# Kernel optimization log

Hardware: AMD Instinct MI355X
Metric: run time of the kernel (lower is better)

## Reference

```python
import jax, jax.numpy as jnp
import numpy as np

NEG_SLOPE = 0.2

def gat_conv(x, src, dst, W, a_src, a_dst, b, num_nodes, concat):
    # PyG GATConv (add_self_loops already applied to src/dst).
    H, C = a_src.shape
    h = (x @ W).reshape(-1, H, C)                      # [N,H,C]
    s = jnp.einsum('nhc,hc->nh', h, a_src)             # per-node src score
    d = jnp.einsum('nhc,hc->nh', h, a_dst)             # per-node dst score
    e = jax.nn.leaky_relu(s[src] + d[dst], NEG_SLOPE)  # [E,H]
    emax = jax.lax.stop_gradient(
        jax.ops.segment_max(e, dst, num_segments=num_nodes))  # [N,H]
    ex = jnp.exp(e - emax[dst])
    denom = jax.ops.segment_sum(ex, dst, num_segments=num_nodes)
    alpha = ex / denom[dst]                            # segment softmax over in-edges
    msg = h[src] * alpha[:, :, None]                   # [E,H,C]
    out = jax.ops.segment_sum(msg, dst, num_segments=num_nodes)
    out = out.reshape(num_nodes, H * C) if concat else out.mean(axis=1)
    return out + b

def setup_inputs() -> dict:
    key = jax.random.key(0)
    ks = jax.random.split(key, 20)
    N, E, F = 50000, 400000, 256
    x = jax.random.normal(ks[0], (N, F), dtype=jnp.float32)
    edge_index = jax.random.randint(ks[1], (2, E), 0, N, dtype=jnp.int64)
    def p(k, shape):
        return (jax.random.normal(k, shape, dtype=jnp.float32) * 0.1)
    inp = {'x': x, 'edge_index': edge_index}
    # conv1: 256 -> 8x32 ; conv2: 256 -> 4x32 ; conv3: 128 -> 2x32 ; conv4: 64 -> 1x32
    dims = [(256, 8, 32), (256, 4, 32), (128, 2, 32), (64, 1, 32)]
    ki = 2
    for i, (fin, H, C) in enumerate(dims, start=1):
        inp[f'W{i}'] = p(ks[ki], (fin, H * C)); ki += 1
        inp[f'a_src{i}'] = p(ks[ki], (H, C)); ki += 1
        inp[f'a_dst{i}'] = p(ks[ki], (H, C)); ki += 1
        bdim = H * C if i < 4 else C
        inp[f'b{i}'] = jnp.zeros((bdim,), dtype=jnp.float32)
    return inp

def reference(x, edge_index, W1, a_src1, a_dst1, b1, W2, a_src2, a_dst2, b2,
              W3, a_src3, a_dst3, b3, W4, a_src4, a_dst4, b4):
    N = x.shape[0]
    loops = jnp.arange(N, dtype=edge_index.dtype)
    src = jnp.concatenate([edge_index[0], loops])
    dst = jnp.concatenate([edge_index[1], loops])
    h = jax.nn.elu(gat_conv(x, src, dst, W1, a_src1, a_dst1, b1, N, True))
    h = jax.nn.elu(gat_conv(h, src, dst, W2, a_src2, a_dst2, b2, N, True))
    h = gat_conv(h, src, dst, W3, a_src3, a_dst3, b3, N, True)
    h = jax.nn.elu(h)
    h = gat_conv(h, src, dst, W4, a_src4, a_dst4, b4, N, False)
    return jax.nn.log_softmax(h, axis=1)
```

## Files before the change

### kernel.cpp

```cpp
#include <hip/hip_runtime.h>
#include <hip/hip_bf16.h>

#define LRELU_SLOPE 0.2f
#define WTOT 108544

typedef __attribute__((ext_vector_type(8))) short short8;
typedef __attribute__((ext_vector_type(4))) float f32x4;

__device__ __forceinline__ unsigned short bf16r(float f) {
    unsigned int u = __builtin_bit_cast(unsigned int, f);
    u += 0x7fffu + ((u >> 16) & 1u);
    return (unsigned short)(u >> 16);
}
__device__ __forceinline__ float bf2f(unsigned short u) {
    return __builtin_bit_cast(float, (unsigned int)u << 16);
}

#define GLD16(g, l)                                                            \
    __builtin_amdgcn_global_load_lds(                                          \
        (const __attribute__((address_space(1))) void*)(g),                    \
        (__attribute__((address_space(3))) void*)(l), 16, 0, 0)

#define QB(v, k) __builtin_amdgcn_ds_swizzle((v), 0x8000 | ((k) * 0x55))


__global__ void k_pre(const float* __restrict__ x, unsigned short* __restrict__ Xb,
                      const float* __restrict__ Wa, const float* __restrict__ Wb,
                      const float* __restrict__ Wc, const float* __restrict__ Wd,
                      unsigned short* __restrict__ Ta, unsigned short* __restrict__ Tb,
                      unsigned short* __restrict__ Tc, unsigned short* __restrict__ Td,
                      const int* __restrict__ ei, int* __restrict__ cnt,
                      int* __restrict__ slot, int XC, int E) {
    int gid = blockIdx.x * blockDim.x + threadIdx.x;
    if (gid < XC) {
        const float4* xp = (const float4*)x + (long)gid * 2;
        float4 a = xp[0], b = xp[1];
        short8 pk;
        pk[0] = (short)bf16r(a.x); pk[1] = (short)bf16r(a.y);
        pk[2] = (short)bf16r(a.z); pk[3] = (short)bf16r(a.w);
        pk[4] = (short)bf16r(b.x); pk[5] = (short)bf16r(b.y);
        pk[6] = (short)bf16r(b.z); pk[7] = (short)bf16r(b.w);
        *(short8*)(Xb + (long)gid * 8) = pk;
        return;
    }
    int id = gid - XC;
    if (id < WTOT) {
        const float* W; unsigned short* T; int K, Nc;
        if (id < 65536)       { W = Wa; T = Ta; K = 256; Nc = 256; }
        else if (id < 98304)  { id -= 65536;  W = Wb; T = Tb; K = 256; Nc = 128; }
        else if (id < 106496) { id -= 98304;  W = Wc; T = Tc; K = 128; Nc = 64; }
        else                  { id -= 106496; W = Wd; T = Td; K = 64;  Nc = 32; }
        int n = id / K, k = id % K;
        T[id] = bf16r(W[(long)k * Nc + n]);
        return;
    }
    int e = id - WTOT;
    if (e >= E) return;
    int dst = ei[E + e];
    slot[e] = atomicAdd(&cnt[dst], 1);
}


__global__ void k_scan_blk(const int* __restrict__ cnt, int* __restrict__ offsR,
                           int* __restrict__ bsum, int* __restrict__ bpre,
                           int* __restrict__ done, int N, int NB) {
    __shared__ int temp[1024];
    __shared__ int last_s;
    int t = threadIdx.x;
    int gi = blockIdx.x * 1024 + t;
    int v = (gi < N) ? cnt[gi] + 1 : 0;
    temp[t] = v;
    __syncthreads();
    for (int o = 1; o < 1024; o <<= 1) {
        int x = (t >= o) ? temp[t - o] : 0;
        __syncthreads();
        temp[t] += x;
        __syncthreads();
    }
    if (gi < N) offsR[gi] = temp[t] - v;
    if (t == 1023) bsum[blockIdx.x] = temp[1023];
    if (t == 0) {
        __threadfence();
        last_s = (atomicAdd(done, 1) == NB - 1) ? 1 : 0;
    }
    __syncthreads();
    if (last_s) {
        __threadfence();
        int v2 = (t < NB) ? bsum[t] : 0;
        temp[t] = v2;
        __syncthreads();
        for (int o = 1; o < 1024; o <<= 1) {
            int x = (t >= o) ? temp[t - o] : 0;
            __syncthreads();
            temp[t] += x;
            __syncthreads();
        }
        if (t < NB) bpre[t] = temp[t] - v2;
        if (t == NB - 1) bpre[NB] = temp[t];
    }
}


__global__ __launch_bounds__(256) void k_mg0fin(
        const int* __restrict__ ei, const int* __restrict__ offsR,
        const int* __restrict__ bpre, const int* __restrict__ slot,
        int* __restrict__ offs, int* __restrict__ adj, int NB, int E,
        const unsigned short* __restrict__ Ab, const unsigned short* __restrict__ WT,
        unsigned short* __restrict__ Cb,
        const float* __restrict__ a_src, const float* __restrict__ a_dst,
        float* __restrict__ sbuf, float* __restrict__ dbuf,
        int M, int RB) {
    constexpr int KT = 256, BN = 64, GX = 4, KH = 128, NR = 2;
    constexpr int KITER = KH / 32;
    constexpr int NBF = BN / 16;
    constexpr int CPR = BN / 32;
    constexpr int SP  = BN + 8;
    constexpr int ASH = 64 * KH;
    constexpr int CHR = KH / 8;
    constexpr int SHC = 4;
    constexpr int AIT = CHR / 4;
    constexpr int BIT = BN * CHR / 256;
    __shared__ __align__(16) unsigned short LB[16384];

    {
        int gtid = blockIdx.x * 256 + threadIdx.x;
        int GT = gridDim.x * 256;
        int N = M;
        int NA = (N + 256) & ~255;
        for (int gi = gtid; gi < NA + E; gi += GT) {
            if (gi < NA) {
                if (gi < N) {
                    int v = offsR[gi] + bpre[gi >> 10];
                    offs[gi] = v;
                    adj[v] = gi;
                } else if (gi == N) {
                    offs[N] = bpre[NB];
                }
            } else {
                int e = gi - NA;
                int dst = ei[E + e];
                adj[offsR[dst] + bpre[dst >> 10] + 1 + slot[e]] = ei[e];
            }
        }
    }

    int id = blockIdx.x;
    int xcd = id & 7;
    int q  = id >> 3;
    int ct = q % GX;
    int rb = (q / GX) * 8 + xcd;
    if (rb >= RB) return;
    int bm = rb * 64, bn = ct * BN;

    int t = threadIdx.x;
    int wv = t >> 6, l = t & 63;
    int row_in = l & 15, quad = l >> 4;
    char* LBb = (char*)LB;
    const char* Agb = (const char*)Ab;
    const char* WTb = (const char*)WT;

    f32x4 acc[NBF];
#pragma unroll
    for (int j = 0; j < NBF; ++j) acc[j] = (f32x4){0.f, 0.f, 0.f, 0.f};

    int arow = wv * 16 + row_in;

#pragma unroll
    for (int r = 0; r < NR; ++r) {
        if (r > 0) __syncthreads();
#pragma unroll
        for (int i = 0; i < AIT; ++i) {
            int c = i * 256 + t;
            int row = c >> SHC;
            int ci  = c & (CHR - 1);
            int cis = ci ^ (row & 7);
            int grow = bm + row; if (grow >= M) grow = M - 1;
            long gb = (long)grow * (KT * 2) + r * (KH * 2) + cis * 16;
            GLD16(Agb + gb, LBb + (i * 256 + wv * 64) * 16);
        }
#pragma unroll
        for (int i = 0; i < BIT; ++i) {
            int c = i * 256 + t;
            int col = c >> SHC;
            int ci  = c & (CHR - 1);
            int cis = ci ^ (col & 7);
            long gb = (long)(bn + col) * (KT * 2) + r * (KH * 2) + cis * 16;
            GLD16(WTb + gb, LBb + ASH * 2 + (i * 256 + wv * 64) * 16);
        }
        asm volatile("s_waitcnt vmcnt(0)" ::: "memory");
        __syncthreads();

#pragma unroll
        for (int ki = 0; ki < KITER; ++ki) {
            int aoff = (arow * (KH * 2) + ki * 64 + quad * 16) ^ ((arow & 7) << 4);
            short8 av = *(const short8*)(LBb + aoff);
#pragma unroll
            for (int f = 0; f < NBF; ++f) {
                int bcol = f * 16 + row_in;
                int boff = ASH * 2 + ((bcol * (KH * 2) + ki * 64 + quad * 16) ^ ((bcol & 7) << 4));
                short8 bv = *(const short8*)(LBb + boff);
                acc[f] = __builtin_amdgcn_mfma_f32_16x16x32_bf16(av, bv, acc[f], 0, 0, 0);
            }
        }
    }
    __syncthreads();

#pragma unroll
    for (int r = 0; r < 4; ++r)
#pragma unroll
        for (int f = 0; f < NBF; ++f)
            LB[(wv * 16 + quad * 4 + r) * SP + f * 16 + row_in] = bf16r(acc[f][r]);
    __syncthreads();

    int rr = t / CPR, cc = t % CPR;
    if (rr < 64) {
        int grow = bm + rr;
        int colb = bn + cc * 32;
        if (grow < M) {
            const unsigned short* ep = &LB[rr * SP + cc * 32];
            short8 v0 = *(const short8*)(ep);
            short8 v1 = *(const short8*)(ep + 8);
            short8 v2 = *(const short8*)(ep + 16);
            short8 v3 = *(const short8*)(ep + 24);
            unsigned short* cp = &Cb[(long)grow * 256 + colb];
            *(short8*)(cp)      = v0;
            *(short8*)(cp + 8)  = v1;
            *(short8*)(cp + 16) = v2;
            *(short8*)(cp + 24) = v3;
            int hd = colb >> 5;
            const float* ap = a_src + hd * 32;
            const float* dp = a_dst + hd * 32;
            float ss = 0.f, dd = 0.f;
#pragma unroll
            for (int u = 0; u < 8; ++u) {
                float va = bf2f((unsigned short)v0[u]); ss += va * ap[u];      dd += va * dp[u];
                float vb = bf2f((unsigned short)v1[u]); ss += vb * ap[8 + u];  dd += vb * dp[8 + u];
                float vc = bf2f((unsigned short)v2[u]); ss += vc * ap[16 + u]; dd += vc * dp[16 + u];
                float vd = bf2f((unsigned short)v3[u]); ss += vd * ap[24 + u]; dd += vd * dp[24 + u];
            }
            sbuf[(long)grow * 8 + hd] = ss;
            dbuf[(long)grow * 8 + hd] = dd;
        }
    }
}


template<int HIN, int NC, int KH>
__global__ __launch_bounds__(256, 4) void k_agmg(
        const unsigned short* __restrict__ h,
        const float* __restrict__ s, const float* __restrict__ dsc,
        const int* __restrict__ offs, const int* __restrict__ adj,
        const float* __restrict__ bias,
        const unsigned short* __restrict__ WT,
        unsigned short* __restrict__ Cb,
        const float* __restrict__ a_src, const float* __restrict__ a_dst,
        float* __restrict__ sb2, float* __restrict__ db2,
        int N, int RB) {
    constexpr int KT   = HIN * 32;
    constexpr int NR   = KT / KH;
    constexpr int KITER = KH / 32;
    constexpr int NBF  = NC / 16;
    constexpr int CPR  = NC / 32;
    constexpr int SP   = NC + 8;
    constexpr int ASH2 = 64 * KT * 2;
    constexpr int CHR  = KH / 8;
    constexpr int BIT  = NC * CHR / 256;
    constexpr int HOUT = NC / 32;
    constexpr int TOT1 = ASH2 + NC * KH * 2;
    constexpr int TOT2 = 64 * SP * 2;
    __shared__ __align__(16) unsigned short LB[(TOT1 > TOT2 ? TOT1 : TOT2) / 2];

    int rb = blockIdx.x;
    if (rb >= RB) return;
    int bm = rb * 64;
    int t = threadIdx.x;
    char* LBb = (char*)LB;

    constexpr int UNITS = 64 * HIN * 4;
    for (int u = t; u < UNITS; u += 256) {
        int c8 = u & 3;
        int hh = (u >> 2) % HIN;
        int nl = u / (4 * HIN);
        int n0 = bm + nl;
        int nn = n0 < N ? n0 : N - 1;
        int beg = offs[nn], end = offs[nn + 1];
        float dn = dsc[nn * HIN + hh];
        int coff = hh * 32 + c8 * 8;
        const unsigned short* hb = h + coff;

        float denom = 0.f;
        float acc[8];
#pragma unroll
        for (int z = 0; z < 8; ++z) acc[z] = 0.f;

        for (int j = beg; j < end; j += 8) {
            int my0 = j + c8;
            int my1 = my0 + 4;
            int i0 = my0 < end ? my0 : end - 1;
            int i1 = my1 < end ? my1 : end - 1;
            int p  = adj[i0];
            int qn = adj[i1];
            int a0 = QB(p, 0),  a1 = QB(p, 1),  a2 = QB(p, 2),  a3 = QB(p, 3);
            int b0 = QB(qn, 0), b1 = QB(qn, 1), b2 = QB(qn, 2), b3 = QB(qn, 3);
            short8 h0 = *(const short8*)(hb + (size_t)a0 * KT);
            short8 h1 = *(const short8*)(hb + (size_t)a1 * KT);
            short8 h2 = *(const short8*)(hb + (size_t)a2 * KT);
            short8 h3 = *(const short8*)(hb + (size_t)a3 * KT);
            short8 h4 = *(const short8*)(hb + (size_t)b0 * KT);
            short8 h5 = *(const short8*)(hb + (size_t)b1 * KT);
            short8 h6 = *(const short8*)(hb + (size_t)b2 * KT);
            short8 h7 = *(const short8*)(hb + (size_t)b3 * KT);
            float e0 = s[p * HIN + hh] + dn;
            float e1 = s[qn * HIN + hh] + dn;
            e0 = e0 > 0.f ? e0 : LRELU_SLOPE * e0;
            e1 = e1 > 0.f ? e1 : LRELU_SLOPE * e1;
            float wA = __expf(fminf(e0, 80.f));
            float wB = __expf(fminf(e1, 80.f));
            if (my0 >= end) wA = 0.f;
            if (my1 >= end) wB = 0.f;
            int wiA = __builtin_bit_cast(int, wA);
            int wiB = __builtin_bit_cast(int, wB);
            float w0 = __builtin_bit_cast(float, QB(wiA, 0));
            float w1 = __builtin_bit_cast(float, QB(wiA, 1));
            float w2 = __builtin_bit_cast(float, QB(wiA, 2));
            float w3 = __builtin_bit_cast(float, QB(wiA, 3));
            float w4 = __builtin_bit_cast(float, QB(wiB, 0));
            float w5 = __builtin_bit_cast(float, QB(wiB, 1));
            float w6 = __builtin_bit_cast(float, QB(wiB, 2));
            float w7 = __builtin_bit_cast(float, QB(wiB, 3));
            denom += ((w0 + w1) + (w2 + w3)) + ((w4 + w5) + (w6 + w7));
#pragma unroll
            for (int z = 0; z < 8; ++z) {
                float aa = w0 * bf2f((unsigned short)h0[z]) + w1 * bf2f((unsigned short)h1[z]);
                float ab = w2 * bf2f((unsigned short)h2[z]) + w3 * bf2f((unsigned short)h3[z]);
                float ac = w4 * bf2f((unsigned short)h4[z]) + w5 * bf2f((unsigned short)h5[z]);
                float ad = w6 * bf2f((unsigned short)h6[z]) + w7 * bf2f((unsigned short)h7[z]);
                acc[z] += (aa + ab) + (ac + ad);
            }
        }

        float inv = 1.0f / denom;
        short8 pk;
#pragma unroll
        for (int z = 0; z < 8; ++z) {
            float o = acc[z] * inv + bias[coff + z];
            float v = o > 0.f ? o : (__expf(o) - 1.f);
            pk[z] = (short)bf16r(v);
        }
        int lbyte = (nl * (KT * 2) + coff * 2) ^ ((nl & 7) << 4);
        *(short8*)(LBb + lbyte) = pk;
    }
    __syncthreads();

    int wv = t >> 6, l = t & 63;
    int row_in = l & 15, quad = l >> 4;
    int arow = wv * 16 + row_in;
    const char* WTb = (const char*)WT;

    f32x4 gac[NBF];
#pragma unroll
    for (int j = 0; j < NBF; ++j) gac[j] = (f32x4){0.f, 0.f, 0.f, 0.f};

#pragma unroll
    for (int r = 0; r < NR; ++r) {
        if (r > 0) __syncthreads();
#pragma unroll
        for (int i = 0; i < BIT; ++i) {
            int c = i * 256 + t;
            int col = c / CHR;
            int ci  = c % CHR;
            int cis = ci ^ (col & 7);
            long gb = (long)col * (KT * 2) + r * (KH * 2) + cis * 16;
            GLD16(WTb + gb, LBb + ASH2 + (i * 256 + wv * 64) * 16);
        }
        asm volatile("s_waitcnt vmcnt(0)" ::: "memory");
        __syncthreads();

#pragma unroll
        for (int ki = 0; ki < KITER; ++ki) {
            int aoff = (arow * (KT * 2) + r * (KH * 2) + ki * 64 + quad * 16) ^ ((arow & 7) << 4);
            short8 av = *(const short8*)(LBb + aoff);
#pragma unroll
            for (int f = 0; f < NBF; ++f) {
                int bcol = f * 16 + row_in;
                int boff = ASH2 + ((bcol * (KH * 2) + ki * 64 + quad * 16) ^ ((bcol & 7) << 4));
                short8 bv = *(const short8*)(LBb + boff);
                gac[f] = __builtin_amdgcn_mfma_f32_16x16x32_bf16(av, bv, gac[f], 0, 0, 0);
            }
        }
    }
    __syncthreads();

#pragma unroll
    for (int r4 = 0; r4 < 4; ++r4)
#pragma unroll
        for (int f = 0; f < NBF; ++f)
            LB[(wv * 16 + quad * 4 + r4) * SP + f * 16 + row_in] = bf16r(gac[f][r4]);
    __syncthreads();

    int rr = t / CPR, cc = t % CPR;
    if (rr < 64) {
        int grow = bm + rr;
        int colb = cc * 32;
        if (grow < N) {
            const unsigned short* ep = &LB[rr * SP + colb];
            short8 v0 = *(const short8*)(ep);
            short8 v1 = *(const short8*)(ep + 8);
            short8 v2 = *(const short8*)(ep + 16);
            short8 v3 = *(const short8*)(ep + 24);
            unsigned short* cp = &Cb[(long)grow * NC + colb];
            *(short8*)(cp)      = v0;
            *(short8*)(cp + 8)  = v1;
            *(short8*)(cp + 16) = v2;
            *(short8*)(cp + 24) = v3;
            int hd = colb >> 5;
            const float* ap = a_src + hd * 32;
            const float* dp = a_dst + hd * 32;
            float ss = 0.f, dd = 0.f;
#pragma unroll
            for (int u = 0; u < 8; ++u) {
                float va = bf2f((unsigned short)v0[u]); ss += va * ap[u];      dd += va * dp[u];
                float vb = bf2f((unsigned short)v1[u]); ss += vb * ap[8 + u];  dd += vb * dp[8 + u];
                float vc = bf2f((unsigned short)v2[u]); ss += vc * ap[16 + u]; dd += vc * dp[16 + u];
                float vd = bf2f((unsigned short)v3[u]); ss += vd * ap[24 + u]; dd += vd * dp[24 + u];
            }
            sb2[(long)grow * HOUT + hd] = ss;
            db2[(long)grow * HOUT + hd] = dd;
        }
    }
}


__global__ void k_aggf_fin(const unsigned short* __restrict__ h, const float* __restrict__ s,
                           const float* __restrict__ dsc, const int* __restrict__ offs,
                           const int* __restrict__ adj, const float* __restrict__ bias,
                           float* __restrict__ out32, int N) {
    const int H = 1, C8 = 4, HC = 32;
    long tid = (long)blockIdx.x * blockDim.x + threadIdx.x;
    if (tid >= (long)N * C8) return;
    int c8 = (int)(tid % C8);
    int n  = (int)(tid / C8);
    int beg = offs[n], end = offs[n + 1];
    float dn = dsc[n * H];
    int coff = c8 * 8;
    const unsigned short* hb = h + coff;

    float denom = 0.f;
    float acc[8];
#pragma unroll
    for (int u = 0; u < 8; ++u) acc[u] = 0.f;

    for (int j = beg; j < end; j += 4) {
        int my = j + c8;
        int idx = my < end ? my : end - 1;
        int sn = adj[idx];
        float e = s[sn * H] + dn;
        e = e > 0.f ? e : LRELU_SLOPE * e;
        float w = __expf(fminf(e, 80.f));
        if (my >= end) w = 0.f;
        int wi = __builtin_bit_cast(int, w);
        int sn0 = QB(sn, 0);
        int sn1 = QB(sn, 1);
        int sn2 = QB(sn, 2);
        int sn3 = QB(sn, 3);
        float w0 = __builtin_bit_cast(float, QB(wi, 0));
        float w1 = __builtin_bit_cast(float, QB(wi, 1));
        float w2 = __builtin_bit_cast(float, QB(wi, 2));
        float w3 = __builtin_bit_cast(float, QB(wi, 3));
        short8 h0 = *(const short8*)(hb + (size_t)sn0 * HC);
        short8 h1 = *(const short8*)(hb + (size_t)sn1 * HC);
        short8 h2 = *(const short8*)(hb + (size_t)sn2 * HC);
        short8 h3 = *(const short8*)(hb + (size_t)sn3 * HC);
        denom += (w0 + w1) + (w2 + w3);
#pragma unroll
        for (int u = 0; u < 8; ++u) {
            float a01 = w0 * bf2f((unsigned short)h0[u]) + w1 * bf2f((unsigned short)h1[u]);
            float a23 = w2 * bf2f((unsigned short)h2[u]) + w3 * bf2f((unsigned short)h3[u]);
            acc[u] += a01 + a23;
        }
    }

    float inv = 1.0f / denom;
    float o[8];
#pragma unroll
    for (int u = 0; u < 8; ++u) o[u] = acc[u] * inv + bias[coff + u];

    float m = o[0];
#pragma unroll
    for (int u = 1; u < 8; ++u) m = fmaxf(m, o[u]);
    m = fmaxf(m, __shfl_xor(m, 1));
    m = fmaxf(m, __shfl_xor(m, 2));
    float ssum = 0.f;
#pragma unroll
    for (int u = 0; u < 8; ++u) ssum += __expf(o[u] - m);
    ssum += __shfl_xor(ssum, 1);
    ssum += __shfl_xor(ssum, 2);
    float lse = m + __logf(ssum);
    float4 lo = {o[0] - lse, o[1] - lse, o[2] - lse, o[3] - lse};
    float4 hi = {o[4] - lse, o[5] - lse, o[6] - lse, o[7] - lse};
    *(float4*)(out32 + tid * 8)     = lo;
    *(float4*)(out32 + tid * 8 + 4) = hi;
}


static inline size_t align_up(size_t x) { return (x + 255) & ~(size_t)255; }

extern "C" void kernel_launch(void* const* d_in, const int* in_sizes, int n_in,
                              void* d_out, int out_size, void* d_ws, size_t ws_size,
                              hipStream_t stream) {
    const float* x   = (const float*)d_in[0];
    const int*   ei  = (const int*)d_in[1];

    const int N = in_sizes[0] / 256;
    const int E = in_sizes[1] / 2;
    const int ET = E + N;
    const int NB = (N + 1023) / 1024;
    const int XC = N * 32;

    size_t off = 0;
    char* ws = (char*)d_ws;
    auto take = [&](size_t bytes) { char* p = ws + off; off += align_up(bytes); return p; };
    int*   cntd  = (int*)take((size_t)(N + 1) * 4);
    int*   offs  = (int*)take((size_t)(N + 1) * 4);
    int*   offsR = (int*)take((size_t)(N + 1) * 4);
    int*   slot  = (int*)take((size_t)E * 4);
    int*   adj   = (int*)take((size_t)ET * 4);
    int*   bsum  = (int*)take((size_t)(NB + 1) * 4);
    int*   bpre  = (int*)take((size_t)(NB + 1) * 4);
    float* s0    = (float*)take((size_t)N * 8 * 4);
    float* d0    = (float*)take((size_t)N * 8 * 4);
    float* s1    = (float*)take((size_t)N * 4 * 4);
    float* d1    = (float*)take((size_t)N * 4 * 4);
    unsigned short* Xb = (unsigned short*)take((size_t)N * 256 * 2);
    unsigned short* Y0 = (unsigned short*)take((size_t)N * 256 * 2);
    unsigned short* Y1 = (unsigned short*)take((size_t)N * 128 * 2);
    unsigned short* WT0 = (unsigned short*)take((size_t)256 * 256 * 2);
    unsigned short* WT1 = (unsigned short*)take((size_t)256 * 128 * 2);
    unsigned short* WT2 = (unsigned short*)take((size_t)128 * 64 * 2);
    unsigned short* WT3 = (unsigned short*)take((size_t)64 * 32 * 2);
    (void)ws_size;

    int* cnt  = cntd;
    int* done = cntd + N;

    const float* as_[4] = {(const float*)d_in[3], (const float*)d_in[7],
                           (const float*)d_in[11], (const float*)d_in[15]};
    const float* ad_[4] = {(const float*)d_in[4], (const float*)d_in[8],
                           (const float*)d_in[12], (const float*)d_in[16]};
    const float* b_[4]  = {(const float*)d_in[5], (const float*)d_in[9],
                           (const float*)d_in[13], (const float*)d_in[17]};

    const int RB  = (N + 63) / 64;
    const int RBp = ((RB + 7) / 8) * 8;

    hipMemsetAsync(cntd, 0, (size_t)(N + 1) * 4, stream);
    {
        long tot = (long)XC + WTOT + E;
        k_pre<<<(int)((tot + 255) / 256), 256, 0, stream>>>(
            x, Xb,
            (const float*)d_in[2], (const float*)d_in[6], (const float*)d_in[10],
            (const float*)d_in[14], WT0, WT1, WT2, WT3, ei, cnt, slot, XC, E);
    }
    k_scan_blk<<<NB, 1024, 0, stream>>>(cnt, offsR, bsum, bpre, done, N, NB);
    k_mg0fin<<<4 * RBp, 256, 0, stream>>>(
        ei, offsR, bpre, slot, offs, adj, NB, E,
        Xb, WT0, Y0, as_[0], ad_[0], s0, d0, N, RB);
    k_agmg<8, 128, 64><<<RB, 256, 0, stream>>>(
        Y0, s0, d0, offs, adj, b_[0], WT1, Y1, as_[1], ad_[1], s1, d1, N, RB);
    k_agmg<4, 64, 128><<<RB, 256, 0, stream>>>(
        Y1, s1, d1, offs, adj, b_[1], WT2, Y0, as_[2], ad_[2], s0, d0, N, RB);
    k_agmg<2, 32, 64><<<RB, 256, 0, stream>>>(
        Y0, s0, d0, offs, adj, b_[2], WT3, Y1, as_[3], ad_[3], s1, d1, N, RB);
    k_aggf_fin<<<(int)(((long)N * 4 + 255) / 256), 256, 0, stream>>>(
        Y1, s1, d1, offs, adj, b_[3], (float*)d_out, N);
}
```

Measured before the change: 298.9 us.

## Split fused aggregate+GEMM into separate aggregation and MFMA GEMM kernels

Replaces the fused per-layer aggregate-then-GEMM kernel with two kernels: a warp-group aggregation kernel that writes the ELU'd bf16 features to global memory, and a standalone MFMA GEMM kernel with an XCD-aware tile mapping that computes the next layer's projections and attention scores. The aim is better occupancy and load balance in the gather phase, since each node is now handled by a small lane group instead of being tied to 64-row GEMM blocks with a large LDS footprint. The cost is an extra global round trip of the intermediate features and extra kernel launches.

Result: no change. 297.1 us (-0.6%).

```diff
diff --git a/kernel.cpp b/kernel.cpp
--- a/kernel.cpp
+++ b/kernel.cpp
@@ -97,6 +97,132 @@
         }
         if (t < NB) bpre[t] = temp[t] - v2;
         if (t == NB - 1) bpre[NB] = temp[t];
+    }
+}
+
+
+template<int BN, int KT, int GX>
+__global__ __launch_bounds__(256) void k_mgemm(const unsigned short* __restrict__ Ab,
+                                               const unsigned short* __restrict__ WT,
+                                               unsigned short* __restrict__ Cb,
+                                               const float* __restrict__ a_src,
+                                               const float* __restrict__ a_dst,
+                                               float* __restrict__ sbuf,
+                                               float* __restrict__ dbuf,
+                                               int M, int Nc, int H, int RB) {
+    constexpr int KH   = (KT == 256) ? 128 : KT;
+    constexpr int NR   = KT / KH;
+    constexpr int KITER = KH / 32;
+    constexpr int NBF = BN / 16;
+    constexpr int CPR = BN / 32;
+    constexpr int SP  = BN + 8;
+    constexpr int ASH = 64 * KH;
+    constexpr int BSH = BN * KH;
+    constexpr int EPIL = 64 * SP;
+    constexpr int LBSZ = (ASH + BSH) > EPIL ? (ASH + BSH) : EPIL;
+    constexpr int CHR = KH / 8;
+    constexpr int SHC = (KH == 128) ? 4 : 3;
+    constexpr int AIT = CHR / 4;
+    constexpr int BIT = BN * CHR / 256;
+    __shared__ __align__(16) unsigned short LB[LBSZ];
+
+    int id = blockIdx.x;
+    int xcd = id & 7;
+    int q  = id >> 3;
+    int ct = q % GX;
+    int rb = (q / GX) * 8 + xcd;
+    if (rb >= RB) return;
+    int bm = rb * 64, bn = ct * BN;
+
+    int t = threadIdx.x;
+    int wv = t >> 6, l = t & 63;
+    int row_in = l & 15, quad = l >> 4;
+    char* LBb = (char*)LB;
+    const char* Agb = (const char*)Ab;
+    const char* WTb = (const char*)WT;
+
+    f32x4 acc[NBF];
+#pragma unroll
+    for (int j = 0; j < NBF; ++j) acc[j] = (f32x4){0.f, 0.f, 0.f, 0.f};
+
+    int arow = wv * 16 + row_in;
+
+#pragma unroll
+    for (int r = 0; r < NR; ++r) {
+        if (r > 0) __syncthreads();
+#pragma unroll
+        for (int i = 0; i < AIT; ++i) {
+            int c = i * 256 + t;
+            int row = c >> SHC;
+            int ci  = c & (CHR - 1);
+            int cis = ci ^ (row & 7);
+            int grow = bm + row; if (grow >= M) grow = M - 1;
+            long gb = (long)grow * (KT * 2) + r * (KH * 2) + cis * 16;
+            GLD16(Agb + gb, LBb + (i * 256 + wv * 64) * 16);
+        }
+#pragma unroll
+        for (int i = 0; i < BIT; ++i) {
+            int c = i * 256 + t;
+            int col = c >> SHC;
+            int ci  = c & (CHR - 1);
+            int cis = ci ^ (col & 7);
+            long gb = (long)(bn + col) * (KT * 2) + r * (KH * 2) + cis * 16;
+            GLD16(WTb + gb, LBb + ASH * 2 + (i * 256 + wv * 64) * 16);
+        }
+        asm volatile("s_waitcnt vmcnt(0)" ::: "memory");
+        __syncthreads();
+
+#pragma unroll
+        for (int ki = 0; ki < KITER; ++ki) {
+            int aoff = (arow * (KH * 2) + ki * 64 + quad * 16) ^ ((arow & 7) << 4);
+            short8 av = *(const short8*)(LBb + aoff);
+#pragma unroll
+            for (int f = 0; f < NBF; ++f) {
+                int bcol = f * 16 + row_in;
+                int boff = ASH * 2 + ((bcol * (KH * 2) + ki * 64 + quad * 16) ^ ((bcol & 7) << 4));
+                short8 bv = *(const short8*)(LBb + boff);
+                acc[f] = __builtin_amdgcn_mfma_f32_16x16x32_bf16(av, bv, acc[f], 0, 0, 0);
+            }
+        }
+    }
+    __syncthreads();
+
+#pragma unroll
+    for (int r = 0; r < 4; ++r)
+#pragma unroll
+        for (int f = 0; f < NBF; ++f)
+            LB[(wv * 16 + quad * 4 + r) * SP + f * 16 + row_in] = bf16r(acc[f][r]);
+    __syncthreads();
+
+    int rr = t / CPR, cc = t % CPR;
+    if (rr < 64) {
+        int grow = bm + rr;
+        int colb = bn + cc * 32;
+        if (grow < M && colb < Nc) {
+            const unsigned short* ep = &LB[rr * SP + cc * 32];
+            short8 v0 = *(const short8*)(ep);
+            short8 v1 = *(const short8*)(ep + 8);
+            short8 v2 = *(const short8*)(ep + 16);
+            short8 v3 = *(const short8*)(ep + 24);
+            unsigned short* cp = &Cb[(long)grow * Nc + colb];
+            *(short8*)(cp)      = v0;
+            *(short8*)(cp + 8)  = v1;
+            *(short8*)(cp + 16) = v2;
+            *(short8*)(cp + 24) = v3;
+            int hd = colb >> 5;
+            const float* ap = a_src + hd * 32;
+            const float* dp = a_dst + hd * 32;
+            float ss = 0.f, dd = 0.f;
+#pragma unroll
+            for (int u = 0; u < 8; ++u) {
+                float va = bf2f((unsigned short)v0[u]); ss += va * ap[u];      dd += va * dp[u];
+                float vb = bf2f((unsigned short)v1[u]); ss += vb * ap[8 + u];  dd += vb * dp[8 + u];
+                float vc = bf2f((unsigned short)v2[u]); ss += vc * ap[16 + u]; dd += vc * dp[16 + u];
+                float vd = bf2f((unsigned short)v3[u]); ss += vd * ap[24 + u]; dd += vd * dp[24 + u];
+            }
+            sbuf[(long)grow * H + hd] = ss;
+            dbuf[(long)grow * H + hd] = dd;
+        }
     }
 }
 
@@ -245,188 +371,78 @@
 }
 
 
-template<int HIN, int NC, int KH>
-__global__ __launch_bounds__(256, 4) void k_agmg(
-        const unsigned short* __restrict__ h,
-        const float* __restrict__ s, const float* __restrict__ dsc,
-        const int* __restrict__ offs, const int* __restrict__ adj,
-        const float* __restrict__ bias,
-        const unsigned short* __restrict__ WT,
-        unsigned short* __restrict__ Cb,
-        const float* __restrict__ a_src, const float* __restrict__ a_dst,
-        float* __restrict__ sb2, float* __restrict__ db2,
-        int N, int RB) {
-    constexpr int KT   = HIN * 32;
-    constexpr int NR   = KT / KH;
-    constexpr int KITER = KH / 32;
-    constexpr int NBF  = NC / 16;
-    constexpr int CPR  = NC / 32;
-    constexpr int SP   = NC + 8;
-    constexpr int ASH2 = 64 * KT * 2;
-    constexpr int CHR  = KH / 8;
-    constexpr int BIT  = NC * CHR / 256;
-    constexpr int HOUT = NC / 32;
-    constexpr int TOT1 = ASH2 + NC * KH * 2;
-    constexpr int TOT2 = 64 * SP * 2;
-    __shared__ __align__(16) unsigned short LB[(TOT1 > TOT2 ? TOT1 : TOT2) / 2];
-
-    int rb = blockIdx.x;
-    if (rb >= RB) return;
-    int bm = rb * 64;
+template<int H>
+__global__ void k_aggw(const unsigned short* __restrict__ h, const float* __restrict__ s,
+                       const float* __restrict__ dsc, const int* __restrict__ offs,
+                       const int* __restrict__ adj, const float* __restrict__ bias,
+                       unsigned short* __restrict__ out16, int N) {
+    constexpr int HC  = H * 32;
+    constexpr int GRP = H * 8;
+    constexpr int NPW = 64 / GRP;
+    constexpr int NPB = 4 * NPW;
     int t = threadIdx.x;
-    char* LBb = (char*)LB;
-
-    constexpr int UNITS = 64 * HIN * 4;
-    for (int u = t; u < UNITS; u += 256) {
-        int c8 = u & 3;
-        int hh = (u >> 2) % HIN;
-        int nl = u / (4 * HIN);
-        int n0 = bm + nl;
-        int nn = n0 < N ? n0 : N - 1;
-        int beg = offs[nn], end = offs[nn + 1];
-        float dn = dsc[nn * HIN + hh];
-        int coff = hh * 32 + c8 * 8;
-        const unsigned short* hb = h + coff;
-
-        float denom = 0.f;
-        float acc[8];
-#pragma unroll
-        for (int z = 0; z < 8; ++z) acc[z] = 0.f;
-
-        for (int j = beg; j < end; j += 8) {
-            int my0 = j + c8;
-            int my1 = my0 + 4;
-            int i0 = my0 < end ? my0 : end - 1;
-            int i1 = my1 < end ? my1 : end - 1;
-            int p  = adj[i0];
-            int qn = adj[i1];
-            int a0 = QB(p, 0),  a1 = QB(p, 1),  a2 = QB(p, 2),  a3 = QB(p, 3);
-            int b0 = QB(qn, 0), b1 = QB(qn, 1), b2 = QB(qn, 2), b3 = QB(qn, 3);
-            short8 h0 = *(const short8*)(hb + (size_t)a0 * KT);
-            short8 h1 = *(const short8*)(hb + (size_t)a1 * KT);
-            short8 h2 = *(const short8*)(hb + (size_t)a2 * KT);
-            short8 h3 = *(const short8*)(hb + (size_t)a3 * KT);
-            short8 h4 = *(const short8*)(hb + (size_t)b0 * KT);
-            short8 h5 = *(const short8*)(hb + (size_t)b1 * KT);
-            short8 h6 = *(const short8*)(hb + (size_t)b2 * KT);
-            short8 h7 = *(const short8*)(hb + (size_t)b3 * KT);
-            float e0 = s[p * HIN + hh] + dn;
-            float e1 = s[qn * HIN + hh] + dn;
-            e0 = e0 > 0.f ? e0 : LRELU_SLOPE * e0;
-            e1 = e1 > 0.f ? e1 : LRELU_SLOPE * e1;
-            float wA = __expf(fminf(e0, 80.f));
-            float wB = __expf(fminf(e1, 80.f));
-            if (my0 >= end) wA = 0.f;
-            if (my1 >= end) wB = 0.f;
-            int wiA = __builtin_bit_cast(int, wA);
-            int wiB = __builtin_bit_cast(int, wB);
-            float w0 = __builtin_bit_cast(float, QB(wiA, 0));
-            float w1 = __builtin_bit_cast(float, QB(wiA, 1));
-            float w2 = __builtin_bit_cast(float, QB(wiA, 2));
-            float w3 = __builtin_bit_cast(float, QB(wiA, 3));
-            float w4 = __builtin_bit_cast(float, QB(wiB, 0));
-            float w5 = __builtin_bit_cast(float, QB(wiB, 1));
-            float w6 = __builtin_bit_cast(float, QB(wiB, 2));
-            float w7 = __builtin_bit_cast(float, QB(wiB, 3));
-            denom += ((w0 + w1) + (w2 + w3)) + ((w4 + w5) + (w6 + w7));
-#pragma unroll
-            for (int z = 0; z < 8; ++z) {
-                float aa = w0 * bf2f((unsigned short)h0[z]) + w1 * bf2f((unsigned short)h1[z]);
-                float ab = w2 * bf2f((unsigned short)h2[z]) + w3 * bf2f((unsigned short)h3[z]);
-                float ac = w4 * bf2f((unsigned short)h4[z]) + w5 * bf2f((unsigned short)h5[z]);
-                float ad = w6 * bf2f((unsigned short)h6[z]) + w7 * bf2f((unsigned short)h7[z]);
-                acc[z] += (aa + ab) + (ac + ad);
-            }
-        }
-
+    int wv = t >> 6, lane = t & 63;
+    int g  = lane / GRP;
+    int gl = lane % GRP;
+    int hh = gl >> 3;
+    int n0 = blockIdx.x * NPB + wv * NPW + g;
+    int n  = n0 < N ? n0 : N - 1;
+    int beg = offs[n], end = offs[n + 1];
+    float dn = dsc[n * H + hh];
+    int coff = gl * 4;
+    const unsigned short* hb = h + coff;
+
+    float denom = 0.f;
+    float a0 = 0.f, a1 = 0.f, a2 = 0.f, a3 = 0.f;
+
+    for (int j = beg; j < end; j += 4) {
+        int i1 = j + 1 < end ? j + 1 : end - 1;
+        int i2 = j + 2 < end ? j + 2 : end - 1;
+        int i3 = j + 3 < end ? j + 3 : end - 1;
+        int sn0 = adj[j];
+        int sn1 = adj[i1];
+        int sn2 = adj[i2];
+        int sn3 = adj[i3];
+        ushort4 h0 = *(const ushort4*)(hb + (size_t)sn0 * HC);
+        ushort4 h1 = *(const ushort4*)(hb + (size_t)sn1 * HC);
+        ushort4 h2 = *(const ushort4*)(hb + (size_t)sn2 * HC);
+        ushort4 h3 = *(const ushort4*)(hb + (size_t)sn3 * HC);
+        float e0 = s[sn0 * H + hh] + dn;
+        float e1 = s[sn1 * H + hh] + dn;
+        float e2 = s[sn2 * H + hh] + dn;
+        float e3 = s[sn3 * H + hh] + dn;
+        e0 = e0 > 0.f ? e0 : LRELU_SLOPE * e0;
+        e1 = e1 > 0.f ? e1 : LRELU_SLOPE * e1;
+        e2 = e2 > 0.f ? e2 : LRELU_SLOPE * e2;
+        e3 = e3 > 0.f ? e3 : LRELU_SLOPE * e3;
+        float w0 = __expf(fminf(e0, 80.f));
+        float w1 = __expf(fminf(e1, 80.f));
+        float w2 = __expf(fminf(e2, 80.f));
+        float w3 = __expf(fminf(e3, 80.f));
+        w1 = j + 1 < end ? w1 : 0.f;
+        w2 = j + 2 < end ? w2 : 0.f;
+        w3 = j + 3 < end ? w3 : 0.f;
+        denom += (w0 + w1) + (w2 + w3);
+        a0 += w0 * bf2f(h0.x) + w1 * bf2f(h1.x) + w2 * bf2f(h2.x) + w3 * bf2f(h3.x);
+        a1 += w0 * bf2f(h0.y) + w1 * bf2f(h1.y) + w2 * bf2f(h2.y) + w3 * bf2f(h3.y);
+        a2 += w0 * bf2f(h0.z) + w1 * bf2f(h1.z) + w2 * bf2f(h2.z) + w3 * bf2f(h3.z);
+        a3 += w0 * bf2f(h0.w) + w1 * bf2f(h1.w) + w2 * bf2f(h2.w) + w3 * bf2f(h3.w);
+    }
+
+    if (n0 < N) {
         float inv = 1.0f / denom;
-        short8 pk;
-#pragma unroll
-        for (int z = 0; z < 8; ++z) {
-            float o = acc[z] * inv + bias[coff + z];
-            float v = o > 0.f ? o : (__expf(o) - 1.f);
-            pk[z] = (short)bf16r(v);
-        }
-        int lbyte = (nl * (KT * 2) + coff * 2) ^ ((nl & 7) << 4);
-        *(short8*)(LBb + lbyte) = pk;
-    }
-    __syncthreads();
-
-    int wv = t >> 6, l = t & 63;
-    int row_in = l & 15, quad = l >> 4;
-    int arow = wv * 16 + row_in;
-    const char* WTb = (const char*)WT;
-
-    f32x4 gac[NBF];
-#pragma unroll
-    for (int j = 0; j < NBF; ++j) gac[j] = (f32x4){0.f, 0.f, 0.f, 0.f};
-
-#pragma unroll
-    for (int r = 0; r < NR; ++r) {
-        if (r > 0) __syncthreads();
-#pragma unroll
-        for (int i = 0; i < BIT; ++i) {
-            int c = i * 256 + t;
-            int col = c / CHR;
-            int ci  = c % CHR;
-            int cis = ci ^ (col & 7);
-            long gb = (long)col * (KT * 2) + r * (KH * 2) + cis * 16;
-            GLD16(WTb + gb, LBb + ASH2 + (i * 256 + wv * 64) * 16);
-        }
-        asm volatile("s_waitcnt vmcnt(0)" ::: "memory");
-        __syncthreads();
-
-#pragma unroll
-        for (int ki = 0; ki < KITER; ++ki) {
-            int aoff = (arow * (KT * 2) + r * (KH * 2) + ki * 64 + quad * 16) ^ ((arow & 7) << 4);
-            short8 av = *(const short8*)(LBb + aoff);
-#pragma unroll
-            for (int f = 0; f < NBF; ++f) {
-                int bcol = f * 16 + row_in;
-                int boff = ASH2 + ((bcol * (KH * 2) + ki * 64 + quad * 16) ^ ((bcol & 7) << 4));
-                short8 bv = *(const short8*)(LBb + boff);
-                gac[f] = __builtin_amdgcn_mfma_f32_16x16x32_bf16(av, bv, gac[f], 0, 0, 0);
-            }
-        }
-    }
-    __syncthreads();
-
-#pragma unroll
-    for (int r4 = 0; r4 < 4; ++r4)
-#pragma unroll
-        for (int f = 0; f < NBF; ++f)
-            LB[(wv * 16 + quad * 4 + r4) * SP + f * 16 + row_in] = bf16r(gac[f][r4]);
-    __syncthreads();
-
-    int rr = t / CPR, cc = t % CPR;
-    if (rr < 64) {
-        int grow = bm + rr;
-        int colb = cc * 32;
-        if (grow < N) {
-            const unsigned short* ep = &LB[rr * SP + colb];
-            short8 v0 = *(const short8*)(ep);
-            short8 v1 = *(const short8*)(ep + 8);
-            short8 v2 = *(const short8*)(ep + 16);
-            short8 v3 = *(const short8*)(ep + 24);
-            unsigned short* cp = &Cb[(long)grow * NC + colb];
-            *(short8*)(cp)      = v0;
-            *(short8*)(cp + 8)  = v1;
-            *(short8*)(cp + 16) = v2;
-            *(short8*)(cp + 24) = v3;
-            int hd = colb >> 5;
-            const float* ap = a_src + hd * 32;
-            const float* dp = a_dst + hd * 32;
-            float ss = 0.f, dd = 0.f;
-#pragma unroll
-            for (int u = 0; u < 8; ++u) {
-                float va = bf2f((unsigned short)v0[u]); ss += va * ap[u];      dd += va * dp[u];
-                float vb = bf2f((unsigned short)v1[u]); ss += vb * ap[8 + u];  dd += vb * dp[8 + u];
-                float vc = bf2f((unsigned short)v2[u]); ss += vc * ap[16 + u]; dd += vc * dp[16 + u];
-                float vd = bf2f((unsigned short)v3[u]); ss += vd * ap[24 + u]; dd += vd * dp[24 + u];
-            }
-            sb2[(long)grow * HOUT + hd] = ss;
-            db2[(long)grow * HOUT + hd] = dd;
-        }
+        const float4 bv = *(const float4*)(bias + coff);
+        float o0 = a0 * inv + bv.x;
+        float o1 = a1 * inv + bv.y;
+        float o2 = a2 * inv + bv.z;
+        float o3 = a3 * inv + bv.w;
+        o0 = o0 > 0.f ? o0 : (__expf(o0) - 1.f);
+        o1 = o1 > 0.f ? o1 : (__expf(o1) - 1.f);
+        o2 = o2 > 0.f ? o2 : (__expf(o2) - 1.f);
+        o3 = o3 > 0.f ? o3 : (__expf(o3) - 1.f);
+        ushort4 pk;
+        pk.x = bf16r(o0); pk.y = bf16r(o1); pk.z = bf16r(o2); pk.w = bf16r(o3);
+        *(ushort4*)(out16 + (size_t)n0 * HC + coff) = pk;
     }
 }
 
@@ -529,11 +545,11 @@
     int*   bpre  = (int*)take((size_t)(NB + 1) * 4);
     float* s0    = (float*)take((size_t)N * 8 * 4);
     float* d0    = (float*)take((size_t)N * 8 * 4);
-    float* s1    = (float*)take((size_t)N * 4 * 4);
-    float* d1    = (float*)take((size_t)N * 4 * 4);
+    float* s1    = (float*)take((size_t)N * 8 * 4);
+    float* d1    = (float*)take((size_t)N * 8 * 4);
     unsigned short* Xb = (unsigned short*)take((size_t)N * 256 * 2);
-    unsigned short* Y0 = (unsigned short*)take((size_t)N * 256 * 2);
-    unsigned short* Y1 = (unsigned short*)take((size_t)N * 128 * 2);
+    unsigned short* Ya = (unsigned short*)take((size_t)N * 256 * 2);
+    unsigned short* Yb = (unsigned short*)take((size_t)N * 256 * 2);
     unsigned short* WT0 = (unsigned short*)take((size_t)256 * 256 * 2);
     unsigned short* WT1 = (unsigned short*)take((size_t)256 * 128 * 2);
     unsigned short* WT2 = (unsigned short*)take((size_t)128 * 64 * 2);
@@ -564,13 +580,16 @@
     k_scan_blk<<<NB, 1024, 0, stream>>>(cnt, offsR, bsum, bpre, done, N, NB);
     k_mg0fin<<<4 * RBp, 256, 0, stream>>>(
         ei, offsR, bpre, slot, offs, adj, NB, E,
-        Xb, WT0, Y0, as_[0], ad_[0], s0, d0, N, RB);
-    k_agmg<8, 128, 64><<<RB, 256, 0, stream>>>(
-        Y0, s0, d0, offs, adj, b_[0], WT1, Y1, as_[1], ad_[1], s1, d1, N, RB);
-    k_agmg<4, 64, 128><<<RB, 256, 0, stream>>>(
-        Y1, s1, d1, offs, adj, b_[1], WT2, Y0, as_[2], ad_[2], s0, d0, N, RB);
-    k_agmg<2, 32, 64><<<RB, 256, 0, stream>>>(
-        Y0, s0, d0, offs, adj, b_[2], WT3, Y1, as_[3], ad_[3], s1, d1, N, RB);
+        Xb, WT0, Ya, as_[0], ad_[0], s0, d0, N, RB);
+    k_aggw<8><<<(N + 3) / 4, 256, 0, stream>>>(Ya, s0, d0, offs, adj, b_[0], Yb, N);
+    k_mgemm<64, 256, 2><<<2 * RBp, 256, 0, stream>>>(
+        Yb, WT1, Ya, as_[1], ad_[1], s1, d1, N, 128, 4, RB);
+    k_aggw<4><<<(N + 7) / 8, 256, 0, stream>>>(Ya, s1, d1, offs, adj, b_[1], Yb, N);
+    k_mgemm<64, 128, 1><<<RBp, 256, 0, stream>>>(
+        Yb, WT2, Ya, as_[2], ad_[2], s0, d0, N, 64, 2, RB);
+    k_aggw<2><<<(N + 15) / 16, 256, 0, stream>>>(Ya, s0, d0, offs, adj, b_[2], Yb, N);
+    k_mgemm<32, 64, 1><<<RBp, 256, 0, stream>>>(
+        Yb, WT3, Ya, as_[3], ad_[3], s1, d1, N, 32, 1, RB);
     k_aggf_fin<<<(int)(((long)N * 4 + 255) / 256), 256, 0, stream>>>(
-        Y1, s1, d1, offs, adj, b_[3], (float*)d_out, N);
-}
+        Ya, s1, d1, offs, adj, b_[3], (float*)d_out, N);
+}
```
